# Kernel tuning notes

Hardware: AMD Instinct MI355X
Metric: run time of the kernel (lower is better)

## Reference

```python
import jax, jax.numpy as jnp
import numpy as np

N = 1048576        # number of time samples (rays)
V = 32             # num_videos
D = 32             # embedding_dim
F = 6              # num_frequencies
K = 2 * F + 1      # basis size: [1, sin(2^j*pi*t), cos(2^j*pi*t)]


def setup_inputs() -> dict:
    key = jax.random.key(0)
    k1, k2, k3 = jax.random.split(key, 3)
    times = jax.random.uniform(k1, (N, 1), dtype=jnp.float32)
    video_ids = jax.random.randint(k2, (N, 1), 0, V, dtype=jnp.int32)
    weights = jax.random.normal(k3, (V, D, K), dtype=jnp.float32)
    return {"times": times, "video_ids": video_ids, "weights": weights}


def _fourier_basis(t):
    # t: [N] -> [N, K] with basis [1, sin(2^j pi t), cos(2^j pi t)] j=0..F-1
    freqs = (2.0 ** jnp.arange(F, dtype=t.dtype)) * jnp.pi  # [F]
    ang = t[:, None] * freqs                                # [N, F]
    return jnp.concatenate(
        [jnp.ones_like(t)[:, None], jnp.sin(ang), jnp.cos(ang)], axis=-1
    )


def reference(times, video_ids, weights):
    shp = times.shape
    t = times.reshape(-1)                       # [N]
    vid = video_ids.reshape(-1).astype(jnp.int32)  # [N]
    basis = _fourier_basis(t)                   # [N, K]
    w = weights[vid]                            # gather: [N, D, K]
    emb = jnp.einsum('ndk,nk->nd', w, basis)    # [N, D]
    return emb.reshape((*shp[:-1], -1))
```

## Files before the change

kernel.cpp:

```cpp
#include <hip/hip_runtime.h>
#include <hip/hip_fp16.h>

#define NRAYS 1048576
#define NV 32
#define ND 32
#define NF 6
#define NK 13
#define RPB 1024
#define NTILE_MAX 96

typedef _Float16 h2 __attribute__((ext_vector_type(2)));
typedef _Float16 h8 __attribute__((ext_vector_type(8)));
typedef float f4 __attribute__((ext_vector_type(4)));

__device__ __forceinline__ h2 pack2(float a, float b) {
#if __has_builtin(__builtin_amdgcn_cvt_pkrtz)
    return __builtin_bit_cast(h2, __builtin_amdgcn_cvt_pkrtz(a, b));
#else
    h2 r; r.x = (_Float16)a; r.y = (_Float16)b; return r;
#endif
}
__device__ __forceinline__ float hwsin(float rev) {
#if __has_builtin(__builtin_amdgcn_sinf)
    return __builtin_amdgcn_sinf(rev);
#else
    return __sinf(6.28318530717958647692f * rev);
#endif
}
__device__ __forceinline__ float hwcos(float rev) {
#if __has_builtin(__builtin_amdgcn_cosf)
    return __builtin_amdgcn_cosf(rev);
#else
    return __cosf(6.28318530717958647692f * rev);
#endif
}

__global__ void pack_weights_kernel(const float* __restrict__ weights,
                                    unsigned* __restrict__ wfrag)
{
    int idx = blockIdx.x * 256 + threadIdx.x;
    if (idx >= 16384) return;
    int v = idx >> 9;
    int r = idx & 511;
    int dhalf = r >> 8;
    int r2 = r & 255;
    int lane = r2 >> 2;
    int e = r2 & 3;
    int d = dhalf * 16 + (lane & 15);
    int k0 = (lane >> 4) * 8 + 2 * e;
    const float* wp = weights + v * (ND * NK) + d * NK;
    float w0 = (k0 < NK) ? wp[k0] : 0.f;
    float w1 = (k0 + 1 < NK) ? wp[k0 + 1] : 0.f;
    wfrag[idx] = __builtin_bit_cast(unsigned, pack2(w0, w1));
}

__global__ __launch_bounds__(256, 4) void VideoEmbedding_kernel(
    const float* __restrict__ times,
    const int* __restrict__ vids,
    const uint4* __restrict__ wfrag,
    float* __restrict__ out)
{
    __shared__ __align__(16) _Float16 s_bt[(RPB + 16) * 16];
    __shared__ unsigned short s_meta[RPB];
    __shared__ int hist[NV];
    __shared__ unsigned ttab[NTILE_MAX];
    __shared__ int s_nT;

    const int tid = threadIdx.x;
    const int rbase = blockIdx.x * RPB;

    if (tid < NV) hist[tid] = 0;
    __syncthreads();

    float t[4];
    int v[4];
#pragma unroll
    for (int it = 0; it < 4; ++it) {
        int lid = it * 256 + tid;
        t[it] = times[rbase + lid];
        v[it] = vids[rbase + lid];
        atomicAdd(&hist[v[it]], 1);
    }
    __syncthreads();

    if (tid < NV) {
        int c = hist[tid];
        int sum = c;
#pragma unroll
        for (int off = 1; off < NV; off <<= 1) {
            int n = __shfl_up(sum, off, NV);
            if (tid >= off) sum += n;
        }
        int excl = sum - c;
        hist[tid] = excl;
        int nt = (c + 15) >> 4;
        int tsum = nt;
#pragma unroll
        for (int off = 1; off < NV; off <<= 1) {
            int n = __shfl_up(tsum, off, NV);
            if (tid >= off) tsum += n;
        }
        int texcl = tsum - nt;
        if (tid == NV - 1) s_nT = tsum;
        unsigned endv = (unsigned)(excl + c);
        for (int s = 0; s < nt; ++s)
            ttab[texcl + s] =
                ((unsigned)tid << 22) | (endv << 11) | (unsigned)(excl + 16 * s);
        uint4 zz; zz.x = zz.y = zz.z = zz.w = 0u;
        *reinterpret_cast<uint4*>(&s_bt[RPB * 16 + tid * 8]) = zz;
    }
    __syncthreads();

#pragma unroll
    for (int it = 0; it < 4; ++it) {
        int slot = atomicAdd(&hist[v[it]], 1);
        s_meta[slot] = (unsigned short)(it * 256 + tid);
        float sv[NF], cv[NF];
        sv[0] = hwsin(0.5f * t[it]);
        cv[0] = hwcos(0.5f * t[it]);
#pragma unroll
        for (int j = 1; j < NF; ++j) {
            float sj = sv[j - 1], cj = cv[j - 1];
            sv[j] = 2.f * sj * cj;
            cv[j] = fmaf(-2.f * sj, sj, 1.f);
        }
        uint4 lo, hi;
        lo.x = __builtin_bit_cast(unsigned, pack2(1.0f, sv[0]));
        lo.y = __builtin_bit_cast(unsigned, pack2(sv[1], sv[2]));
        lo.z = __builtin_bit_cast(unsigned, pack2(sv[3], sv[4]));
        lo.w = __builtin_bit_cast(unsigned, pack2(sv[5], cv[0]));
        hi.x = __builtin_bit_cast(unsigned, pack2(cv[1], cv[2]));
        hi.y = __builtin_bit_cast(unsigned, pack2(cv[3], cv[4]));
        hi.z = __builtin_bit_cast(unsigned, pack2(cv[5], 0.0f));
        hi.w = 0u;
        uint4* bt = reinterpret_cast<uint4*>(&s_bt[slot * 16]);
        bt[0] = lo;
        bt[1] = hi;
    }
    __syncthreads();

    const int wid = tid >> 6;
    const int lane = tid & 63;
    const int lrow = lane & 15;
    const int lkc = lane >> 4;
    const int T = s_nT;

    for (int tt = wid; tt < T; tt += 4) {
        const unsigned e = ttab[tt];
        const int rowstart = (int)(e & 0x7FFu);
        const int rend = (int)((e >> 11) & 0x7FFu);
        const int vv = (int)(e >> 22);

        h8 a = *reinterpret_cast<const h8*>(
            &s_bt[(rowstart + lrow) * 16 + lkc * 8]);
        uint4 b0u = wfrag[(vv * 2 + 0) * 64 + lane];
        uint4 b1u = wfrag[(vv * 2 + 1) * 64 + lane];

        f4 z = {0.f, 0.f, 0.f, 0.f};
        f4 c0 = __builtin_amdgcn_mfma_f32_16x16x32_f16(
            a, __builtin_bit_cast(h8, b0u), z, 0, 0, 0);
        f4 c1 = __builtin_amdgcn_mfma_f32_16x16x32_f16(
            a, __builtin_bit_cast(h8, b1u), z, 0, 0, 0);

#pragma unroll
        for (int j = 0; j < 4; ++j) {
            const int srow = rowstart + lkc * 4 + j;
            if (srow < rend) {
                const int lidx = s_meta[srow];
                float* o = out + (size_t)(rbase + lidx) * 32 + lrow;
                o[0] = c0[j];
                o[16] = c1[j];
            }
        }
    }
}

extern "C" void kernel_launch(void* const* d_in, const int* in_sizes, int n_in,
                              void* d_out, int out_size, void* d_ws, size_t ws_size,
                              hipStream_t stream) {
    const float* times = (const float*)d_in[0];
    const int* vids = (const int*)d_in[1];
    const float* weights = (const float*)d_in[2];
    float* out = (float*)d_out;
    unsigned* wfrag = (unsigned*)d_ws;

    hipLaunchKernelGGL(pack_weights_kernel, dim3(64), dim3(256), 0, stream,
                       weights, wfrag);
    hipLaunchKernelGGL(VideoEmbedding_kernel, dim3(1024), dim3(256), 0, stream,
                       times, vids, (const uint4*)wfrag, out);
}
```

Baseline: 36.75 us.

## Stage MFMA results in LDS and write output rows coalesced in original order

Cuts rays per block from 1024 to 256 and launches four times as many blocks. MFMA outputs are no longer scattered straight to global memory through the sorted permutation. They go into an fp16 LDS buffer, and a final pass writes each original row with contiguous 16-byte float4 stores. This aims to replace strided scattered 4-byte stores with coalesced writes, at the cost of an extra LDS round trip, an extra barrier, and rounding the fp32 accumulators to fp16 before output.

```diff
diff --git a/kernel.cpp b/kernel.cpp
--- a/kernel.cpp
+++ b/kernel.cpp
@@ -6,8 +6,8 @@
 #define ND 32
 #define NF 6
 #define NK 13
-#define RPB 1024
-#define NTILE_MAX 96
+#define RPB 256
+#define NTILE_MAX 64
 
 typedef _Float16 h2 __attribute__((ext_vector_type(2)));
 typedef _Float16 h8 __attribute__((ext_vector_type(8)));
@@ -60,8 +60,9 @@
     const uint4* __restrict__ wfrag,
     float* __restrict__ out)
 {
-    __shared__ __align__(16) _Float16 s_bt[(RPB + 16) * 16];
-    __shared__ unsigned short s_meta[RPB];
+    __shared__ __align__(16) _Float16 s_bt[(RPB + 16) * 32];
+    __shared__ __align__(16) _Float16 s_c[RPB * 32];
+    __shared__ unsigned short s_inv[RPB];
     __shared__ int hist[NV];
     __shared__ unsigned ttab[NTILE_MAX];
     __shared__ int s_nT;
@@ -72,15 +73,9 @@
     if (tid < NV) hist[tid] = 0;
     __syncthreads();
 
-    float t[4];
-    int v[4];
-#pragma unroll
-    for (int it = 0; it < 4; ++it) {
-        int lid = it * 256 + tid;
-        t[it] = times[rbase + lid];
-        v[it] = vids[rbase + lid];
-        atomicAdd(&hist[v[it]], 1);
-    }
+    const float t = times[rbase + tid];
+    const int vid = vids[rbase + tid];
+    atomicAdd(&hist[vid], 1);
     __syncthreads();
 
     if (tid < NV) {
@@ -106,25 +101,26 @@
         for (int s = 0; s < nt; ++s)
             ttab[texcl + s] =
                 ((unsigned)tid << 22) | (endv << 11) | (unsigned)(excl + 16 * s);
+    }
+    if (tid < 64) {
         uint4 zz; zz.x = zz.y = zz.z = zz.w = 0u;
-        *reinterpret_cast<uint4*>(&s_bt[RPB * 16 + tid * 8]) = zz;
-    }
-    __syncthreads();
-
-#pragma unroll
-    for (int it = 0; it < 4; ++it) {
-        int slot = atomicAdd(&hist[v[it]], 1);
-        s_meta[slot] = (unsigned short)(it * 256 + tid);
+        reinterpret_cast<uint4*>(s_bt + RPB * 32)[tid] = zz;
+    }
+    __syncthreads();
+
+    {
+        int slot = atomicAdd(&hist[vid], 1);
+        s_inv[tid] = (unsigned short)slot;
         float sv[NF], cv[NF];
-        sv[0] = hwsin(0.5f * t[it]);
-        cv[0] = hwcos(0.5f * t[it]);
+        sv[0] = hwsin(0.5f * t);
+        cv[0] = hwcos(0.5f * t);
 #pragma unroll
         for (int j = 1; j < NF; ++j) {
             float sj = sv[j - 1], cj = cv[j - 1];
             sv[j] = 2.f * sj * cj;
             cv[j] = fmaf(-2.f * sj, sj, 1.f);
         }
-        uint4 lo, hi;
+        uint4 lo, hi, zz;
         lo.x = __builtin_bit_cast(unsigned, pack2(1.0f, sv[0]));
         lo.y = __builtin_bit_cast(unsigned, pack2(sv[1], sv[2]));
         lo.z = __builtin_bit_cast(unsigned, pack2(sv[3], sv[4]));
@@ -133,26 +129,28 @@
         hi.y = __builtin_bit_cast(unsigned, pack2(cv[3], cv[4]));
         hi.z = __builtin_bit_cast(unsigned, pack2(cv[5], 0.0f));
         hi.w = 0u;
-        uint4* bt = reinterpret_cast<uint4*>(&s_bt[slot * 16]);
-        bt[0] = lo;
-        bt[1] = hi;
-    }
-    __syncthreads();
-
-    const int wid = tid >> 6;
+        zz.x = zz.y = zz.z = zz.w = 0u;
+        uint4* row = reinterpret_cast<uint4*>(s_bt + slot * 32);
+        row[0] = lo;
+        row[1] = hi;
+        row[2] = zz;
+        row[3] = zz;
+    }
+    __syncthreads();
+
     const int lane = tid & 63;
     const int lrow = lane & 15;
     const int lkc = lane >> 4;
     const int T = s_nT;
 
-    for (int tt = wid; tt < T; tt += 4) {
+    for (int tt = tid >> 6; tt < T; tt += 4) {
         const unsigned e = ttab[tt];
         const int rowstart = (int)(e & 0x7FFu);
         const int rend = (int)((e >> 11) & 0x7FFu);
         const int vv = (int)(e >> 22);
 
         h8 a = *reinterpret_cast<const h8*>(
-            &s_bt[(rowstart + lrow) * 16 + lkc * 8]);
+            &s_bt[(rowstart + lrow) * 32 + lkc * 8]);
         uint4 b0u = wfrag[(vv * 2 + 0) * 64 + lane];
         uint4 b1u = wfrag[(vv * 2 + 1) * 64 + lane];
 
@@ -166,12 +164,29 @@
         for (int j = 0; j < 4; ++j) {
             const int srow = rowstart + lkc * 4 + j;
             if (srow < rend) {
-                const int lidx = s_meta[srow];
-                float* o = out + (size_t)(rbase + lidx) * 32 + lrow;
-                o[0] = c0[j];
-                o[16] = c1[j];
+                s_c[srow * 32 + lrow] = (_Float16)c0[j];
+                s_c[srow * 32 + lrow + 16] = (_Float16)c1[j];
             }
         }
+    }
+    __syncthreads();
+
+    const int q = tid & 7;
+    const int g = tid >> 3;
+#pragma unroll
+    for (int p = 0; p < 8; ++p) {
+        const int r = p * 32 + g;
+        const int slot = s_inv[r];
+        const uint2 cw =
+            *reinterpret_cast<const uint2*>(&s_c[slot * 32 + q * 4]);
+        const h2 p0 = __builtin_bit_cast(h2, cw.x);
+        const h2 p1 = __builtin_bit_cast(h2, cw.y);
+        f4 res;
+        res.x = (float)p0.x;
+        res.y = (float)p0.y;
+        res.z = (float)p1.x;
+        res.w = (float)p1.y;
+        reinterpret_cast<f4*>(out)[(size_t)(rbase + r) * 8 + q] = res;
     }
 }
 
@@ -186,6 +201,6 @@
 
     hipLaunchKernelGGL(pack_weights_kernel, dim3(64), dim3(256), 0, stream,
                        weights, wfrag);
-    hipLaunchKernelGGL(VideoEmbedding_kernel, dim3(1024), dim3(256), 0, stream,
+    hipLaunchKernelGGL(VideoEmbedding_kernel, dim3(4096), dim3(256), 0, stream,
                        times, vids, (const uint4*)wfrag, out);
 }
```

After: 46.81 us. 1.27x slower.
